# Performance work log

Hardware: AMD Instinct MI355X
Metric: run time of the kernel (lower is better)

## Reference

```python
import jax, jax.numpy as jnp
import numpy as np

N, INC, MID, K = 65536, 256, 64, 16
EPS = 1e-5  # BatchNorm1d default eps


def _bn(x, g, b, m, v):
    # eval-mode BatchNorm1d applied per-channel along the last dim
    return (x - m) * (g * jax.lax.rsqrt(v + EPS)) + b


def setup_inputs() -> dict:
    key = jax.random.key(0)
    ks = jax.random.split(key, 40)
    rn = lambda i, shape, s=0.05: (jax.random.normal(ks[i], shape, jnp.float32) * s)
    pv = lambda i, n: jax.random.uniform(ks[i], (n,), jnp.float32, 0.5, 1.5)  # positive running var
    return {
        "feats": jax.random.normal(ks[0], (N, INC), jnp.float32),
        "pos": jax.random.uniform(ks[1], (N, 3), jnp.float32) * 10.0,
        "idx": jax.random.randint(ks[2], (N, K), 0, N),
        "w_in": rn(3, (MID, INC)),
        "w_q": rn(4, (MID, MID)), "b_q": rn(5, (MID,)),
        "w_k": rn(6, (MID, MID)), "b_k": rn(7, (MID,)),
        "w_v": rn(8, (MID, MID)), "b_v": rn(9, (MID,)),
        # pos_enc: Linear(3,3) -> BN(3) -> ReLU -> Linear(3,mid) -> BN(mid) -> ReLU
        "pe_w1": rn(10, (3, 3)), "pe_b1": rn(11, (3,)),
        "pe_g1": jnp.ones(3), "pe_be1": rn(12, (3,)), "pe_m1": rn(13, (3,)), "pe_v1": pv(14, 3),
        "pe_w2": rn(15, (MID, 3)), "pe_b2": rn(16, (MID,)),
        "pe_g2": jnp.ones(MID), "pe_be2": rn(17, (MID,)), "pe_m2": rn(18, (MID,)), "pe_v2": pv(19, MID),
        # mlp_gamma: Linear(mid,mid) -> BN(mid) -> ReLU -> Linear(mid,mid) -> BN(mid) -> ReLU
        "ga_w1": rn(20, (MID, MID)), "ga_b1": rn(21, (MID,)),
        "ga_g1": jnp.ones(MID), "ga_be1": rn(22, (MID,)), "ga_m1": rn(23, (MID,)), "ga_v1": pv(24, MID),
        "ga_w2": rn(25, (MID, MID)), "ga_b2": rn(26, (MID,)),
        "ga_g2": jnp.ones(MID), "ga_be2": rn(27, (MID,)), "ga_m2": rn(28, (MID,)), "ga_v2": pv(29, MID),
        "w_out": rn(30, (INC, MID)),
    }


def reference(feats, pos, w_in, w_q, b_q, w_k, b_k, w_v, b_v,
              pe_w1, pe_b1, pe_g1, pe_be1, pe_m1, pe_v1,
              pe_w2, pe_b2, pe_g2, pe_be2, pe_m2, pe_v2,
              ga_w1, ga_b1, ga_g1, ga_be1, ga_m1, ga_v1,
              ga_w2, ga_b2, ga_g2, ga_be2, ga_m2, ga_v2,
              w_out, idx):
    xx = feats @ w_in.T                              # [N, mid]
    q = xx @ w_q.T + b_q
    k = xx @ w_k.T + b_k
    v = xx @ w_v.T + b_v
    xv = v[idx]                                      # [N, K, mid] gather
    xk = k[idx]                                      # [N, K, mid]
    xpos = pos[idx]                                  # [N, K, 3]
    # pos_enc
    p = jax.nn.relu(_bn(xpos @ pe_w1.T + pe_b1, pe_g1, pe_be1, pe_m1, pe_v1))
    p = jax.nn.relu(_bn(p @ pe_w2.T + pe_b2, pe_g2, pe_be2, pe_m2, pe_v2))  # [N, K, mid]
    # vector attention logits
    w = xk - q[:, None, :] + p                       # [N, K, mid]
    # mlp_gamma
    w = jax.nn.relu(_bn(w @ ga_w1.T + ga_b1, ga_g1, ga_be1, ga_m1, ga_v1))
    w = jax.nn.relu(_bn(w @ ga_w2.T + ga_b2, ga_g2, ga_be2, ga_m2, ga_v2))
    w = jax.nn.softmax(w, axis=1)                    # softmax over neighbors
    out = jnp.sum((xv + p) * w, axis=1)              # [N, mid]
    out = out @ w_out.T                              # [N, inc]
    return out + feats
```

## Files before the change

### kernel.cpp

```cpp
#include <hip/hip_runtime.h>

#define NPTS 65536
#define INC  256
#define MID  64
#define KNB  16
#define WSTR 72

#define WIN_S   0
#define WQ_S    16384
#define WK_S    20480
#define WV_S    24576
#define GA1_S   28672
#define GA2_S   32768
#define WOUT_S  36864
#define NFRAG_ENT 6656
#define BQ1F_S  53248

#define LOG2E 1.44269504088896340736f

typedef __attribute__((ext_vector_type(8))) short short8;
typedef __attribute__((ext_vector_type(4))) float f32x4;

#define MFMA(a, b, c) __builtin_amdgcn_mfma_f32_16x16x32_bf16((a), (b), (c), 0, 0, 0)
#define WBAR() __builtin_amdgcn_wave_barrier()

__device__ inline float bf2f(unsigned short s) {
    unsigned int u = ((unsigned int)s) << 16;
    return __builtin_bit_cast(float, u);
}
__device__ inline unsigned int pk_bf16(float lo, float hi) {
    unsigned int r;
    asm("v_cvt_pk_bf16_f32 %0, %1, %2" : "=v"(r) : "v"(lo), "v"(hi));
    return r;
}
__device__ inline short f2bf(float f) { return (short)pk_bf16(f, f); }
__device__ inline float exp2fast(float x) {
    float r;
    asm("v_exp_f32 %0, %1" : "=v"(r) : "v"(x));
    return r;
}

__device__ inline short8 cvtf8(f32x4 a, f32x4 b) {
    union { unsigned int u[4]; short8 s; } r;
    r.u[0] = pk_bf16(a[0], a[1]); r.u[1] = pk_bf16(a[2], a[3]);
    r.u[2] = pk_bf16(b[0], b[1]); r.u[3] = pk_bf16(b[2], b[3]);
    return r.s;
}
__device__ inline short8 load_cvt8(const float* __restrict__ p) {
    const f32x4* v = (const f32x4*)p;
    return cvtf8(v[0], v[1]);
}
__device__ inline short8 load_cvt8s(const float* __restrict__ p, float scale) {
    const f32x4* v = (const f32x4*)p;
    f32x4 a = v[0], b = v[1];
    #pragma unroll
    for (int i = 0; i < 4; i++) { a[i] *= scale; b[i] *= scale; }
    return cvtf8(a, b);
}

__global__ __launch_bounds__(256) void k_prep(
    const float* __restrict__ w_in, const float* __restrict__ w_q,
    const float* __restrict__ w_k, const float* __restrict__ w_v,
    const float* __restrict__ ga_w1, const float* __restrict__ ga_w2,
    const float* __restrict__ w_out, const float* __restrict__ b_q,
    const float* __restrict__ ga_g1, const float* __restrict__ ga_v1,
    const float* __restrict__ ga_b1, const float* __restrict__ ga_be1,
    const float* __restrict__ ga_m1,
    const float* __restrict__ ga_g2, const float* __restrict__ ga_v2,
    short* __restrict__ wbuf)
{
    int gid = blockIdx.x * 256 + threadIdx.x;
    if (gid >= NFRAG_ENT + 64) return;
    if (gid < 2048) {
        int e = gid, f = e >> 6, ln = e & 63;
        int nt = f & 3, ks = f >> 2;
        int row = nt * 16 + (ln & 15), col = ks * 32 + (ln >> 4) * 8;
        *(short8*)&wbuf[(size_t)gid * 8] = load_cvt8(w_in + (size_t)row * INC + col);
    } else if (gid < 4608) {
        int seg = (gid - 2048) >> 9;
        int e = (gid - 2048) & 511;
        int f = e >> 6, ln = e & 63;
        int nt = f & 3, ks = f >> 2;
        int row = nt * 16 + (ln & 15), col = ks * 32 + (ln >> 4) * 8;
        if (seg == 0) {
            float s1r = ga_g1[row] * rsqrtf(ga_v1[row] + 1e-5f);
            float accv[8];
            #pragma unroll
            for (int o = 0; o < 8; o++) accv[o] = 0.f;
            for (int c = 0; c < 64; c++) {
                float a = ga_w1[(size_t)row * MID + c] * s1r;
                #pragma unroll
                for (int o = 0; o < 8; o++)
                    accv[o] += a * w_q[(size_t)c * MID + col + o];
            }
            f32x4 lo = {accv[0], accv[1], accv[2], accv[3]};
            f32x4 hi = {accv[4], accv[5], accv[6], accv[7]};
            *(short8*)&wbuf[(size_t)gid * 8] = cvtf8(lo, hi);
        } else {
            const float* m = seg == 1 ? w_k : seg == 2 ? w_v
                           : seg == 3 ? ga_w1 : ga_w2;
            float scale = 1.f;
            if (seg == 3)      scale = ga_g1[row] * rsqrtf(ga_v1[row] + 1e-5f);
            else if (seg == 4) scale = ga_g2[row] * rsqrtf(ga_v2[row] + 1e-5f) * LOG2E;
            *(short8*)&wbuf[(size_t)gid * 8] = load_cvt8s(m + (size_t)row * MID + col, scale);
        }
    } else if (gid < NFRAG_ENT) {
        int e = gid - 4608, f = e >> 6, ln = e & 63;
        int nt = f >> 1, ks = f & 1;
        int row = nt * 16 + (ln & 15), col = ks * 32 + (ln >> 4) * 8;
        *(short8*)&wbuf[(size_t)gid * 8] = load_cvt8(w_out + (size_t)row * MID + col);
    } else {
        int ch = gid - NFRAG_ENT;
        float s1r = ga_g1[ch] * rsqrtf(ga_v1[ch] + 1e-5f);
        float acc = 0.f;
        for (int c = 0; c < 64; c++) acc += ga_w1[(size_t)ch * MID + c] * b_q[c];
        float beta1 = (ga_b1[ch] - ga_m1[ch]) * s1r + ga_be1[ch];
        ((float*)(wbuf + BQ1F_S))[ch] = s1r * acc - beta1;
    }
}

__global__ __launch_bounds__(256) void k_qkv(
    const float* __restrict__ feats, const short* __restrict__ wfrag,
    const float* __restrict__ pos,
    const float* __restrict__ b_k, const float* __restrict__ b_v,
    const float* __restrict__ pe_w1, const float* __restrict__ pe_b1,
    const float* __restrict__ pe_g1, const float* __restrict__ pe_be1,
    const float* __restrict__ pe_m1, const float* __restrict__ pe_v1,
    const float* __restrict__ pe_w2, const float* __restrict__ pe_b2,
    const float* __restrict__ pe_g2, const float* __restrict__ pe_be2,
    const float* __restrict__ pe_m2, const float* __restrict__ pe_v2,
    short* __restrict__ q1f_out, unsigned* __restrict__ kv_out)
{
    __shared__ __align__(16) short XL[4][16 * WSTR];
    __shared__ float PS[4][16 * 4];
    const int tid = threadIdx.x;
    const int wave = tid >> 6, lane = tid & 63;
    const int l15 = lane & 15, quad = lane >> 4;
    const int rb = (blockIdx.x * 4 + wave) * 16;

    if (lane < 16) {
        float s0 = pe_g1[0] * rsqrtf(pe_v1[0] + 1e-5f);
        float s1 = pe_g1[1] * rsqrtf(pe_v1[1] + 1e-5f);
        float sc = pe_g1[2] * rsqrtf(pe_v1[2] + 1e-5f);
        float px = pos[(size_t)(rb + lane) * 3 + 0];
        float py = pos[(size_t)(rb + lane) * 3 + 1];
        float pz = pos[(size_t)(rb + lane) * 3 + 2];
        PS[wave][lane * 4 + 0] =
            fmaxf((px * pe_w1[0] + py * pe_w1[1] + pz * pe_w1[2] + pe_b1[0] - pe_m1[0]) * s0 + pe_be1[0], 0.f);
        PS[wave][lane * 4 + 1] =
            fmaxf((px * pe_w1[3] + py * pe_w1[4] + pz * pe_w1[5] + pe_b1[1] - pe_m1[1]) * s1 + pe_be1[1], 0.f);
        PS[wave][lane * 4 + 2] =
            fmaxf((px * pe_w1[6] + py * pe_w1[7] + pz * pe_w1[8] + pe_b1[2] - pe_m1[2]) * sc + pe_be1[2], 0.f);
    }

    const float* bq1f = (const float*)(wfrag + BQ1F_S);
    float w2c0[4], w2c1[4], w2c2[4], s2c[4], sh2c[4], bq1c[4], bkc[4], bvc[4];
    #pragma unroll
    for (int nt = 0; nt < 4; nt++) {
        int ch = nt * 16 + l15;
        w2c0[nt] = pe_w2[ch * 3 + 0]; w2c1[nt] = pe_w2[ch * 3 + 1]; w2c2[nt] = pe_w2[ch * 3 + 2];
        float s2 = pe_g2[ch] * rsqrtf(pe_v2[ch] + 1e-5f);
        s2c[nt] = s2;
        sh2c[nt] = (pe_b2[ch] - pe_m2[ch]) * s2 + pe_be2[ch];
        bq1c[nt] = bq1f[ch];
        bkc[nt] = b_k[ch]; bvc[nt] = b_v[ch];
    }

    f32x4 acc[4];
    #pragma unroll
    for (int nt = 0; nt < 4; nt++) acc[nt] = (f32x4){0.f, 0.f, 0.f, 0.f};
    const float* arow = feats + (size_t)(rb + l15) * INC + quad * 8;
    #pragma unroll
    for (int ks = 0; ks < 8; ks++) {
        short8 a = load_cvt8(arow + ks * 32);
        #pragma unroll
        for (int nt = 0; nt < 4; nt++) {
            short8 b = *(const short8*)&wfrag[WIN_S + (size_t)((ks * 4 + nt) * 64 + lane) * 8];
            acc[nt] = MFMA(a, b, acc[nt]);
        }
    }
    #pragma unroll
    for (int nt = 0; nt < 4; nt++) {
        unsigned int p01 = pk_bf16(acc[nt][0], acc[nt][1]);
        unsigned int p23 = pk_bf16(acc[nt][2], acc[nt][3]);
        XL[wave][(quad * 4 + 0) * WSTR + nt * 16 + l15] = (short)p01;
        XL[wave][(quad * 4 + 1) * WSTR + nt * 16 + l15] = (short)(p01 >> 16);
        XL[wave][(quad * 4 + 2) * WSTR + nt * 16 + l15] = (short)p23;
        XL[wave][(quad * 4 + 3) * WSTR + nt * 16 + l15] = (short)(p23 >> 16);
    }
    WBAR();
    short8 a0 = *(const short8*)&XL[wave][l15 * WSTR + quad * 8];
    short8 a1 = *(const short8*)&XL[wave][l15 * WSTR + 32 + quad * 8];
    WBAR();

    float p10[4], p11[4], p12[4];
    #pragma unroll
    for (int r = 0; r < 4; r++) {
        p10[r] = PS[wave][(quad * 4 + r) * 4 + 0];
        p11[r] = PS[wave][(quad * 4 + r) * 4 + 1];
        p12[r] = PS[wave][(quad * 4 + r) * 4 + 2];
    }
    float pe_[4][4];
    #pragma unroll
    for (int nt = 0; nt < 4; nt++)
        #pragma unroll
        for (int r = 0; r < 4; r++)
            pe_[nt][r] = fmaxf((p10[r] * w2c0[nt] + p11[r] * w2c1[nt] + p12[r] * w2c2[nt])
                               * s2c[nt] + sh2c[nt], 0.f);

    #pragma unroll
    for (int nt = 0; nt < 4; nt++) {
        short8 b0 = *(const short8*)&wfrag[WQ_S + (size_t)((nt) * 64 + lane) * 8];
        short8 b1 = *(const short8*)&wfrag[WQ_S + (size_t)((4 + nt) * 64 + lane) * 8];
        f32x4 c = (f32x4){0.f, 0.f, 0.f, 0.f};
        c = MFMA(a0, b0, c); c = MFMA(a1, b1, c);
        unsigned int p01 = pk_bf16(c[0] + bq1c[nt], c[1] + bq1c[nt]);
        unsigned int p23 = pk_bf16(c[2] + bq1c[nt], c[3] + bq1c[nt]);
        q1f_out[(unsigned)(rb + quad * 4 + 0) * 64u + nt * 16 + l15] = (short)p01;
        q1f_out[(unsigned)(rb + quad * 4 + 1) * 64u + nt * 16 + l15] = (short)(p01 >> 16);
        q1f_out[(unsigned)(rb + quad * 4 + 2) * 64u + nt * 16 + l15] = (short)p23;
        q1f_out[(unsigned)(rb + quad * 4 + 3) * 64u + nt * 16 + l15] = (short)(p23 >> 16);
    }

    WBAR();
    #pragma unroll
    for (int nt = 0; nt < 4; nt++) {
        short8 b0 = *(const short8*)&wfrag[WK_S + (size_t)((nt) * 64 + lane) * 8];
        short8 b1 = *(const short8*)&wfrag[WK_S + (size_t)((4 + nt) * 64 + lane) * 8];
        f32x4 c = (f32x4){0.f, 0.f, 0.f, 0.f};
        c = MFMA(a0, b0, c); c = MFMA(a1, b1, c);
        unsigned int p01 = pk_bf16(c[0] + bkc[nt] + pe_[nt][0], c[1] + bkc[nt] + pe_[nt][1]);
        unsigned int p23 = pk_bf16(c[2] + bkc[nt] + pe_[nt][2], c[3] + bkc[nt] + pe_[nt][3]);
        XL[wave][(quad * 4 + 0) * WSTR + nt * 16 + l15] = (short)p01;
        XL[wave][(quad * 4 + 1) * WSTR + nt * 16 + l15] = (short)(p01 >> 16);
        XL[wave][(quad * 4 + 2) * WSTR + nt * 16 + l15] = (short)p23;
        XL[wave][(quad * 4 + 3) * WSTR + nt * 16 + l15] = (short)(p23 >> 16);
    }
    WBAR();
    short8 ak0 = *(const short8*)&XL[wave][l15 * WSTR + quad * 8];
    short8 ak1 = *(const short8*)&XL[wave][l15 * WSTR + 32 + quad * 8];
    WBAR();
    float k1f[4][4];
    #pragma unroll
    for (int nt = 0; nt < 4; nt++) {
        short8 b0 = *(const short8*)&wfrag[GA1_S + (size_t)((nt) * 64 + lane) * 8];
        short8 b1 = *(const short8*)&wfrag[GA1_S + (size_t)((4 + nt) * 64 + lane) * 8];
        f32x4 c = (f32x4){0.f, 0.f, 0.f, 0.f};
        c = MFMA(ak0, b0, c); c = MFMA(ak1, b1, c);
        #pragma unroll
        for (int r = 0; r < 4; r++) k1f[nt][r] = c[r];
    }

    #pragma unroll
    for (int nt = 0; nt < 4; nt++) {
        short8 b0 = *(const short8*)&wfrag[WV_S + (size_t)((nt) * 64 + lane) * 8];
        short8 b1 = *(const short8*)&wfrag[WV_S + (size_t)((4 + nt) * 64 + lane) * 8];
        f32x4 c = (f32x4){0.f, 0.f, 0.f, 0.f};
        c = MFMA(a0, b0, c); c = MFMA(a1, b1, c);
        #pragma unroll
        for (int r = 0; r < 4; r++) {
            float vv = c[r] + bvc[nt] + pe_[nt][r];
            kv_out[(unsigned)(rb + quad * 4 + r) * 64u + nt * 16 + l15] =
                pk_bf16(k1f[nt][r], vv);
        }
    }
}

#define GATHER(KVN, IT2)                                                      \
    _Pragma("unroll")                                                         \
    for (int j = 0; j < KNB; j++) {                                           \
        int mj = __builtin_amdgcn_readlane(m_all, (IT2) * 16 + j);            \
        KVN[j] = kvbuf[(unsigned)mj * 64u + (unsigned)lane];                  \
    }

#define ATTN_POINT(IT, KV, QV, WB)                                            \
    {                                                                         \
        short* wb_ = (WB);                                                    \
        _Pragma("unroll")                                                     \
        for (int j = 0; j < KNB; j += 2) {                                    \
            float h0 = fmaxf(__builtin_bit_cast(float, KV[j] << 16) - (QV), 0.f);     \
            float h1 = fmaxf(__builtin_bit_cast(float, KV[j + 1] << 16) - (QV), 0.f); \
            unsigned pkw = pk_bf16(h0, h1);                                   \
            wb_[(j) * WSTR + lane] = (short)pkw;                              \
            wb_[(j + 1) * WSTR + lane] = (short)(pkw >> 16);                  \
        }                                                                     \
        short8 c0 = *(const short8*)&wb_[l15 * WSTR + quad * 8];              \
        short8 c1 = *(const short8*)&wb_[l15 * WSTR + 32 + quad * 8];         \
        float smv[4][4];                                                      \
        _Pragma("unroll")                                                     \
        for (int nt = 0; nt < 4; nt++) {                                      \
            short8 b0 = *(const short8*)&BW[(size_t)((nt) * 64 + lane) * 8];  \
            short8 b1 = *(const short8*)&BW[(size_t)((4 + nt) * 64 + lane) * 8]; \
            f32x4 c = (f32x4){0.f, 0.f, 0.f, 0.f};                            \
            c = MFMA(c0, b0, c); c = MFMA(c1, b1, c);                         \
            _Pragma("unroll")                                                 \
            for (int r = 0; r < 4; r++)                                       \
                smv[nt][r] = fmaxf(c[r] + b2c[nt], 0.f);                      \
        }                                                                     \
        float sarr[4];                                                        \
        _Pragma("unroll")                                                     \
        for (int nt = 0; nt < 4; nt++) {                                      \
            float e0 = exp2fast(smv[nt][0]), e1 = exp2fast(smv[nt][1]);       \
            float e2 = exp2fast(smv[nt][2]), e3 = exp2fast(smv[nt][3]);       \
            float s = e0 + e1 + e2 + e3;                                      \
            s += __shfl_xor(s, 16);                                           \
            s += __shfl_xor(s, 32);                                           \
            sarr[nt] = s;                                                     \
            unsigned p01 = pk_bf16(e0, e1);                                   \
            unsigned p23 = pk_bf16(e2, e3);                                   \
            wb_[(quad * 4 + 0) * WSTR + nt * 16 + l15] = (short)p01;          \
            wb_[(quad * 4 + 1) * WSTR + nt * 16 + l15] = (short)(p01 >> 16);  \
            wb_[(quad * 4 + 2) * WSTR + nt * 16 + l15] = (short)p23;          \
            wb_[(quad * 4 + 3) * WSTR + nt * 16 + l15] = (short)(p23 >> 16);  \
        }                                                                     \
        float oacc = 0.f;                                                     \
        _Pragma("unroll")                                                     \
        for (int j = 0; j < KNB; j++)                                         \
            oacc += __builtin_bit_cast(float, KV[j] & 0xffff0000u)            \
                    * bf2f((unsigned short)wb_[j * WSTR + lane]);             \
        float s01 = (quad == 0) ? sarr[0] : sarr[1];                          \
        float s23 = (quad == 2) ? sarr[2] : sarr[3];                          \
        float ssel = (quad < 2) ? s01 : s23;                                  \
        OM[((IT) * 4 + wave) * WSTR + lane] = f2bf(oacc * (1.0f / ssel));     \
    }

__global__ __launch_bounds__(256) void k_attn(
    const int* __restrict__ idx,
    const unsigned short* __restrict__ q1f,
    const unsigned* __restrict__ kvbuf, const short* __restrict__ wfrag,
    const float* __restrict__ ga_b2, const float* __restrict__ ga_g2,
    const float* __restrict__ ga_be2, const float* __restrict__ ga_m2,
    const float* __restrict__ ga_v2,
    const float* __restrict__ feats, float* __restrict__ out)
{
    __shared__ __align__(16) short BW[512 * 8];
    __shared__ __align__(16) short Wb[4][2][16 * WSTR];
    __shared__ __align__(16) short OM[16 * WSTR];
    const int tid = threadIdx.x;
    const int wave = tid >> 6, lane = tid & 63;
    const int l15 = lane & 15, quad = lane >> 4;

    #pragma unroll
    for (int rep = 0; rep < 2; rep++) {
        int e = rep * 256 + tid;
        *(short8*)&BW[(size_t)e * 8] = *(const short8*)&wfrag[GA2_S + (size_t)e * 8];
    }

    float b2c[4];
    #pragma unroll
    for (int nt = 0; nt < 4; nt++) {
        int ch = nt * 16 + l15;
        float s2 = ga_g2[ch] * rsqrtf(ga_v2[ch] + 1e-5f);
        b2c[nt] = (ga_b2[ch] * s2 + ga_be2[ch] - ga_m2[ch] * s2) * LOG2E;
    }

    const int n0 = blockIdx.x * 16 + wave;
    int m_all = idx[(unsigned)(n0 + (lane >> 4) * 4) * 16u + (unsigned)(lane & 15)];
    float qf0 = bf2f(q1f[(unsigned)(n0     ) * 64u + lane]);
    float qf1 = bf2f(q1f[(unsigned)(n0 +  4) * 64u + lane]);
    float qf2 = bf2f(q1f[(unsigned)(n0 +  8) * 64u + lane]);
    float qf3 = bf2f(q1f[(unsigned)(n0 + 12) * 64u + lane]);
    __syncthreads();

    unsigned kvA[KNB], kvB[KNB];
    GATHER(kvA, 0)
    GATHER(kvB, 1)
    ATTN_POINT(0, kvA, qf0, &Wb[wave][0][0])
    GATHER(kvA, 2)
    ATTN_POINT(1, kvB, qf1, &Wb[wave][1][0])
    GATHER(kvB, 3)
    ATTN_POINT(2, kvA, qf2, &Wb[wave][0][0])
    ATTN_POINT(3, kvB, qf3, &Wb[wave][1][0])

    __syncthreads();
    short8 A0 = *(const short8*)&OM[l15 * WSTR + quad * 8];
    short8 A1 = *(const short8*)&OM[l15 * WSTR + 32 + quad * 8];
    const int rb = blockIdx.x * 16;
    #pragma unroll
    for (int t = 0; t < 4; t++) {
        int nt = wave * 4 + t;
        short8 b0 = *(const short8*)&wfrag[WOUT_S + (size_t)((nt * 2 + 0) * 64 + lane) * 8];
        short8 b1 = *(const short8*)&wfrag[WOUT_S + (size_t)((nt * 2 + 1) * 64 + lane) * 8];
        f32x4 c = (f32x4){0.f, 0.f, 0.f, 0.f};
        c = MFMA(A0, b0, c);
        c = MFMA(A1, b1, c);
        #pragma unroll
        for (int r = 0; r < 4; r++) {
            size_t off = (size_t)(rb + quad * 4 + r) * INC + nt * 16 + l15;
            out[off] = c[r] + feats[off];
        }
    }
}

extern "C" void kernel_launch(void* const* d_in, const int* in_sizes, int n_in,
                              void* d_out, int out_size, void* d_ws, size_t ws_size,
                              hipStream_t stream)
{
    const float* feats = (const float*)d_in[0];
    const float* pos   = (const float*)d_in[1];
    const int*   idx   = (const int*)d_in[2];
    const float* w_in  = (const float*)d_in[3];
    const float* w_q   = (const float*)d_in[4];
    const float* b_q   = (const float*)d_in[5];
    const float* w_k   = (const float*)d_in[6];
    const float* b_k   = (const float*)d_in[7];
    const float* w_v   = (const float*)d_in[8];
    const float* b_v   = (const float*)d_in[9];
    const float* pe_w1 = (const float*)d_in[10];
    const float* pe_b1 = (const float*)d_in[11];
    const float* pe_g1 = (const float*)d_in[12];
    const float* pe_be1= (const float*)d_in[13];
    const float* pe_m1 = (const float*)d_in[14];
    const float* pe_v1 = (const float*)d_in[15];
    const float* pe_w2 = (const float*)d_in[16];
    const float* pe_b2 = (const float*)d_in[17];
    const float* pe_g2 = (const float*)d_in[18];
    const float* pe_be2= (const float*)d_in[19];
    const float* pe_m2 = (const float*)d_in[20];
    const float* pe_v2 = (const float*)d_in[21];
    const float* ga_w1 = (const float*)d_in[22];
    const float* ga_b1 = (const float*)d_in[23];
    const float* ga_g1 = (const float*)d_in[24];
    const float* ga_be1= (const float*)d_in[25];
    const float* ga_m1 = (const float*)d_in[26];
    const float* ga_v1 = (const float*)d_in[27];
    const float* ga_w2 = (const float*)d_in[28];
    const float* ga_b2 = (const float*)d_in[29];
    const float* ga_g2 = (const float*)d_in[30];
    const float* ga_be2= (const float*)d_in[31];
    const float* ga_m2 = (const float*)d_in[32];
    const float* ga_v2 = (const float*)d_in[33];
    const float* w_out = (const float*)d_in[34];

    char* ws = (char*)d_ws;
    short*    q1f  = (short*)(ws);
    unsigned* kv   = (unsigned*)(ws + (size_t) 8 * 1024 * 1024);
    short*    wbuf = (short*)(ws + (size_t)24 * 1024 * 1024);

    k_prep<<<27, 256, 0, stream>>>(w_in, w_q, w_k, w_v, ga_w1, ga_w2, w_out, b_q,
                                   ga_g1, ga_v1, ga_b1, ga_be1, ga_m1,
                                   ga_g2, ga_v2, wbuf);
    k_qkv<<<NPTS / 64, 256, 0, stream>>>(feats, wbuf, pos, b_k, b_v,
                                         pe_w1, pe_b1, pe_g1, pe_be1, pe_m1, pe_v1,
                                         pe_w2, pe_b2, pe_g2, pe_be2, pe_m2, pe_v2,
                                         q1f, kv);
    k_attn<<<NPTS / 16, 256, 0, stream>>>(idx,
                                          (const unsigned short*)q1f, kv, wbuf,
                                          ga_b2, ga_g2, ga_be2, ga_m2, ga_v2,
                                          feats, (float*)d_out);
}
```

Measured before the change: 246.3 us.

## Split each k_qkv row tile across two waves by output-column halves

k_qkv now assigns each 16-row tile to a pair of waves, each computing half of the 64 output channels, so a block covers 32 rows and the grid doubles. The intermediate xx and k tiles are shared through LDS with block-wide barriers instead of per-wave barriers. This is meant to raise parallelism and cut per-wave register pressure and serial MFMA chains. The cost is that feats rows are loaded and converted twice, plus block-level synchronization.

```diff
diff --git a/kernel.cpp b/kernel.cpp
--- a/kernel.cpp
+++ b/kernel.cpp
@@ -131,137 +131,147 @@
     const float* __restrict__ pe_m2, const float* __restrict__ pe_v2,
     short* __restrict__ q1f_out, unsigned* __restrict__ kv_out)
 {
-    __shared__ __align__(16) short XL[4][16 * WSTR];
-    __shared__ float PS[4][16 * 4];
+    __shared__ __align__(16) short XLa[2][16 * WSTR];
+    __shared__ __align__(16) short XLb[2][16 * WSTR];
+    __shared__ float PS[2][16 * 4];
     const int tid = threadIdx.x;
     const int wave = tid >> 6, lane = tid & 63;
     const int l15 = lane & 15, quad = lane >> 4;
-    const int rb = (blockIdx.x * 4 + wave) * 16;
-
-    if (lane < 16) {
+    const int tile = wave >> 1;
+    const int half = wave & 1;
+    const int nt0 = half * 2;
+    const int rb = (blockIdx.x * 2 + tile) * 16;
+
+    if (half == 0 && lane < 16) {
         float s0 = pe_g1[0] * rsqrtf(pe_v1[0] + 1e-5f);
         float s1 = pe_g1[1] * rsqrtf(pe_v1[1] + 1e-5f);
         float sc = pe_g1[2] * rsqrtf(pe_v1[2] + 1e-5f);
         float px = pos[(size_t)(rb + lane) * 3 + 0];
         float py = pos[(size_t)(rb + lane) * 3 + 1];
         float pz = pos[(size_t)(rb + lane) * 3 + 2];
-        PS[wave][lane * 4 + 0] =
+        PS[tile][lane * 4 + 0] =
             fmaxf((px * pe_w1[0] + py * pe_w1[1] + pz * pe_w1[2] + pe_b1[0] - pe_m1[0]) * s0 + pe_be1[0], 0.f);
-        PS[wave][lane * 4 + 1] =
+        PS[tile][lane * 4 + 1] =
             fmaxf((px * pe_w1[3] + py * pe_w1[4] + pz * pe_w1[5] + pe_b1[1] - pe_m1[1]) * s1 + pe_be1[1], 0.f);
-        PS[wave][lane * 4 + 2] =
+        PS[tile][lane * 4 + 2] =
             fmaxf((px * pe_w1[6] + py * pe_w1[7] + pz * pe_w1[8] + pe_b1[2] - pe_m1[2]) * sc + pe_be1[2], 0.f);
     }
 
     const float* bq1f = (const float*)(wfrag + BQ1F_S);
-    float w2c0[4], w2c1[4], w2c2[4], s2c[4], sh2c[4], bq1c[4], bkc[4], bvc[4];
-    #pragma unroll
-    for (int nt = 0; nt < 4; nt++) {
-        int ch = nt * 16 + l15;
-        w2c0[nt] = pe_w2[ch * 3 + 0]; w2c1[nt] = pe_w2[ch * 3 + 1]; w2c2[nt] = pe_w2[ch * 3 + 2];
+    float w2c0[2], w2c1[2], w2c2[2], s2c[2], sh2c[2], bq1c[2], bkc[2], bvc[2];
+    #pragma unroll
+    for (int i = 0; i < 2; i++) {
+        int ch = (nt0 + i) * 16 + l15;
+        w2c0[i] = pe_w2[ch * 3 + 0]; w2c1[i] = pe_w2[ch * 3 + 1]; w2c2[i] = pe_w2[ch * 3 + 2];
         float s2 = pe_g2[ch] * rsqrtf(pe_v2[ch] + 1e-5f);
-        s2c[nt] = s2;
-        sh2c[nt] = (pe_b2[ch] - pe_m2[ch]) * s2 + pe_be2[ch];
-        bq1c[nt] = bq1f[ch];
-        bkc[nt] = b_k[ch]; bvc[nt] = b_v[ch];
-    }
-
-    f32x4 acc[4];
-    #pragma unroll
-    for (int nt = 0; nt < 4; nt++) acc[nt] = (f32x4){0.f, 0.f, 0.f, 0.f};
+        s2c[i] = s2;
+        sh2c[i] = (pe_b2[ch] - pe_m2[ch]) * s2 + pe_be2[ch];
+        bq1c[i] = bq1f[ch];
+        bkc[i] = b_k[ch]; bvc[i] = b_v[ch];
+    }
+
+    f32x4 acc[2];
+    #pragma unroll
+    for (int i = 0; i < 2; i++) acc[i] = (f32x4){0.f, 0.f, 0.f, 0.f};
     const float* arow = feats + (size_t)(rb + l15) * INC + quad * 8;
     #pragma unroll
     for (int ks = 0; ks < 8; ks++) {
         short8 a = load_cvt8(arow + ks * 32);
         #pragma unroll
-        for (int nt = 0; nt < 4; nt++) {
-            short8 b = *(const short8*)&wfrag[WIN_S + (size_t)((ks * 4 + nt) * 64 + lane) * 8];
-            acc[nt] = MFMA(a, b, acc[nt]);
+        for (int i = 0; i < 2; i++) {
+            short8 b = *(const short8*)&wfrag[WIN_S + (size_t)((ks * 4 + nt0 + i) * 64 + lane) * 8];
+            acc[i] = MFMA(a, b, acc[i]);
         }
     }
     #pragma unroll
-    for (int nt = 0; nt < 4; nt++) {
-        unsigned int p01 = pk_bf16(acc[nt][0], acc[nt][1]);
-        unsigned int p23 = pk_bf16(acc[nt][2], acc[nt][3]);
-        XL[wave][(quad * 4 + 0) * WSTR + nt * 16 + l15] = (short)p01;
-        XL[wave][(quad * 4 + 1) * WSTR + nt * 16 + l15] = (short)(p01 >> 16);
-        XL[wave][(quad * 4 + 2) * WSTR + nt * 16 + l15] = (short)p23;
-        XL[wave][(quad * 4 + 3) * WSTR + nt * 16 + l15] = (short)(p23 >> 16);
-    }
-    WBAR();
-    short8 a0 = *(const short8*)&XL[wave][l15 * WSTR + quad * 8];
-    short8 a1 = *(const short8*)&XL[wave][l15 * WSTR + 32 + quad * 8];
-    WBAR();
+    for (int i = 0; i < 2; i++) {
+        unsigned int p01 = pk_bf16(acc[i][0], acc[i][1]);
+        unsigned int p23 = pk_bf16(acc[i][2], acc[i][3]);
+        int cb = (nt0 + i) * 16 + l15;
+        XLa[tile][(quad * 4 + 0) * WSTR + cb] = (short)p01;
+        XLa[tile][(quad * 4 + 1) * WSTR + cb] = (short)(p01 >> 16);
+        XLa[tile][(quad * 4 + 2) * WSTR + cb] = (short)p23;
+        XLa[tile][(quad * 4 + 3) * WSTR + cb] = (short)(p23 >> 16);
+    }
+    __syncthreads();
+
+    short8 a0 = *(const short8*)&XLa[tile][l15 * WSTR + quad * 8];
+    short8 a1 = *(const short8*)&XLa[tile][l15 * WSTR + 32 + quad * 8];
 
     float p10[4], p11[4], p12[4];
     #pragma unroll
     for (int r = 0; r < 4; r++) {
-        p10[r] = PS[wave][(quad * 4 + r) * 4 + 0];
-        p11[r] = PS[wave][(quad * 4 + r) * 4 + 1];
-        p12[r] = PS[wave][(quad * 4 + r) * 4 + 2];
-    }
-    float pe_[4][4];
-    #pragma unroll
-    for (int nt = 0; nt < 4; nt++)
+        p10[r] = PS[tile][(quad * 4 + r) * 4 + 0];
+        p11[r] = PS[tile][(quad * 4 + r) * 4 + 1];
+        p12[r] = PS[tile][(quad * 4 + r) * 4 + 2];
+    }
+    float pe_[2][4];
+    #pragma unroll
+    for (int i = 0; i < 2; i++)
         #pragma unroll
         for (int r = 0; r < 4; r++)
-            pe_[nt][r] = fmaxf((p10[r] * w2c0[nt] + p11[r] * w2c1[nt] + p12[r] * w2c2[nt])
-                               * s2c[nt] + sh2c[nt], 0.f);
-
-    #pragma unroll
-    for (int nt = 0; nt < 4; nt++) {
+            pe_[i][r] = fmaxf((p10[r] * w2c0[i] + p11[r] * w2c1[i] + p12[r] * w2c2[i])
+                               * s2c[i] + sh2c[i], 0.f);
+
+    #pragma unroll
+    for (int i = 0; i < 2; i++) {
+        int nt = nt0 + i;
         short8 b0 = *(const short8*)&wfrag[WQ_S + (size_t)((nt) * 64 + lane) * 8];
         short8 b1 = *(const short8*)&wfrag[WQ_S + (size_t)((4 + nt) * 64 + lane) * 8];
         f32x4 c = (f32x4){0.f, 0.f, 0.f, 0.f};
         c = MFMA(a0, b0, c); c = MFMA(a1, b1, c);
-        unsigned int p01 = pk_bf16(c[0] + bq1c[nt], c[1] + bq1c[nt]);
-        unsigned int p23 = pk_bf16(c[2] + bq1c[nt], c[3] + bq1c[nt]);
+        unsigned int p01 = pk_bf16(c[0] + bq1c[i], c[1] + bq1c[i]);
+        unsigned int p23 = pk_bf16(c[2] + bq1c[i], c[3] + bq1c[i]);
         q1f_out[(unsigned)(rb + quad * 4 + 0) * 64u + nt * 16 + l15] = (short)p01;
         q1f_out[(unsigned)(rb + quad * 4 + 1) * 64u + nt * 16 + l15] = (short)(p01 >> 16);
         q1f_out[(unsigned)(rb + quad * 4 + 2) * 64u + nt * 16 + l15] = (short)p23;
         q1f_out[(unsigned)(rb + quad * 4 + 3) * 64u + nt * 16 + l15] = (short)(p23 >> 16);
     }
 
-    WBAR();
-    #pragma unroll
-    for (int nt = 0; nt < 4; nt++) {
+    #pragma unroll
+    for (int i = 0; i < 2; i++) {
+        int nt = nt0 + i;
         short8 b0 = *(const short8*)&wfrag[WK_S + (size_t)((nt) * 64 + lane) * 8];
         short8 b1 = *(const short8*)&wfrag[WK_S + (size_t)((4 + nt) * 64 + lane) * 8];
         f32x4 c = (f32x4){0.f, 0.f, 0.f, 0.f};
         c = MFMA(a0, b0, c); c = MFMA(a1, b1, c);
-        unsigned int p01 = pk_bf16(c[0] + bkc[nt] + pe_[nt][0], c[1] + bkc[nt] + pe_[nt][1]);
-        unsigned int p23 = pk_bf16(c[2] + bkc[nt] + pe_[nt][2], c[3] + bkc[nt] + pe_[nt][3]);
-        XL[wave][(quad * 4 + 0) * WSTR + nt * 16 + l15] = (short)p01;
-        XL[wave][(quad * 4 + 1) * WSTR + nt * 16 + l15] = (short)(p01 >> 16);
-        XL[wave][(quad * 4 + 2) * WSTR + nt * 16 + l15] = (short)p23;
-        XL[wave][(quad * 4 + 3) * WSTR + nt * 16 + l15] = (short)(p23 >> 16);
-    }
-    WBAR();
-    short8 ak0 = *(const short8*)&XL[wave][l15 * WSTR + quad * 8];
-    short8 ak1 = *(const short8*)&XL[wave][l15 * WSTR + 32 + quad * 8];
-    WBAR();
-    float k1f[4][4];
-    #pragma unroll
-    for (int nt = 0; nt < 4; nt++) {
+        unsigned int p01 = pk_bf16(c[0] + bkc[i] + pe_[i][0], c[1] + bkc[i] + pe_[i][1]);
+        unsigned int p23 = pk_bf16(c[2] + bkc[i] + pe_[i][2], c[3] + bkc[i] + pe_[i][3]);
+        int cb = nt * 16 + l15;
+        XLb[tile][(quad * 4 + 0) * WSTR + cb] = (short)p01;
+        XLb[tile][(quad * 4 + 1) * WSTR + cb] = (short)(p01 >> 16);
+        XLb[tile][(quad * 4 + 2) * WSTR + cb] = (short)p23;
+        XLb[tile][(quad * 4 + 3) * WSTR + cb] = (short)(p23 >> 16);
+    }
+    __syncthreads();
+
+    short8 ak0 = *(const short8*)&XLb[tile][l15 * WSTR + quad * 8];
+    short8 ak1 = *(const short8*)&XLb[tile][l15 * WSTR + 32 + quad * 8];
+
+    float k1f[2][4];
+    #pragma unroll
+    for (int i = 0; i < 2; i++) {
+        int nt = nt0 + i;
         short8 b0 = *(const short8*)&wfrag[GA1_S + (size_t)((nt) * 64 + lane) * 8];
         short8 b1 = *(const short8*)&wfrag[GA1_S + (size_t)((4 + nt) * 64 + lane) * 8];
         f32x4 c = (f32x4){0.f, 0.f, 0.f, 0.f};
         c = MFMA(ak0, b0, c); c = MFMA(ak1, b1, c);
         #pragma unroll
-        for (int r = 0; r < 4; r++) k1f[nt][r] = c[r];
-    }
-
-    #pragma unroll
-    for (int nt = 0; nt < 4; nt++) {
+        for (int r = 0; r < 4; r++) k1f[i][r] = c[r];
+    }
+
+    #pragma unroll
+    for (int i = 0; i < 2; i++) {
+        int nt = nt0 + i;
         short8 b0 = *(const short8*)&wfrag[WV_S + (size_t)((nt) * 64 + lane) * 8];
         short8 b1 = *(const short8*)&wfrag[WV_S + (size_t)((4 + nt) * 64 + lane) * 8];
         f32x4 c = (f32x4){0.f, 0.f, 0.f, 0.f};
         c = MFMA(a0, b0, c); c = MFMA(a1, b1, c);
         #pragma unroll
         for (int r = 0; r < 4; r++) {
-            float vv = c[r] + bvc[nt] + pe_[nt][r];
+            float vv = c[r] + bvc[i] + pe_[i][r];
             kv_out[(unsigned)(rb + quad * 4 + r) * 64u + nt * 16 + l15] =
-                pk_bf16(k1f[nt][r], vv);
+                pk_bf16(k1f[i][r], vv);
         }
     }
 }
@@ -440,7 +450,7 @@
     k_prep<<<27, 256, 0, stream>>>(w_in, w_q, w_k, w_v, ga_w1, ga_w2, w_out, b_q,
                                    ga_g1, ga_v1, ga_b1, ga_be1, ga_m1,
                                    ga_g2, ga_v2, wbuf);
-    k_qkv<<<NPTS / 64, 256, 0, stream>>>(feats, wbuf, pos, b_k, b_v,
+    k_qkv<<<NPTS / 32, 256, 0, stream>>>(feats, wbuf, pos, b_k, b_v,
                                          pe_w1, pe_b1, pe_g1, pe_be1, pe_m1, pe_v1,
                                          pe_w2, pe_b2, pe_g2, pe_be2, pe_m2, pe_v2,
                                          q1f, kv);
```

New measurement: 254.5 us. +3.3%, slower.
